# Kernel optimization log

Measured on AMD Instinct MI355X. Metric: run time of the kernel, lower is better.

Reference implementation:

```python
import jax, jax.numpy as jnp
import numpy as np

T, NP, NA, NV = 8, 16000, 16000, 200
DIN, H, KA, L = 256, 256, 4, 5
YEARS_TRAIN = (5, 6, 7)
BETA, EPS = 0.5, 1.0
SQRT2 = 1.4142135623730951


def setup_inputs() -> dict:
    key = jax.random.key(0)
    ks = jax.random.split(key, 24)
    s = 0.05
    return {
        'x_paper': jax.random.normal(ks[0], (T, NP, DIN), jnp.float32),
        'x_author': jax.random.normal(ks[1], (T, NA, DIN), jnp.float32),
        'x_venue': jax.random.normal(ks[2], (T, NV, DIN), jnp.float32),
        'neigh_author_idx': jax.random.randint(ks[3], (NP, KA), 0, NA),
        'neigh_venue_idx': jax.random.randint(ks[4], (NP,), 0, NV),
        'y_true': jax.random.uniform(ks[5], (len(YEARS_TRAIN), NP, L), jnp.float32, 0.0, 50.0),
        'W_paper': s * jax.random.normal(ks[6], (DIN, H), jnp.float32),
        'b_paper': jnp.zeros((H,), jnp.float32),
        'W_author': s * jax.random.normal(ks[7], (DIN, H), jnp.float32),
        'b_author': jnp.zeros((H,), jnp.float32),
        'W_venue': s * jax.random.normal(ks[8], (DIN, H), jnp.float32),
        'b_venue': jnp.zeros((H,), jnp.float32),
        'w_meta': jax.random.normal(ks[9], (3,), jnp.float32),
        'Wx': s * jax.random.normal(ks[10], (H, 3 * H), jnp.float32),
        'Wh': s * jax.random.normal(ks[11], (H, 3 * H), jnp.float32),
        'b_gru': jnp.zeros((3 * H,), jnp.float32),
        'W_eta': s * jax.random.normal(ks[12], (H, 1), jnp.float32),
        'b_eta': jnp.zeros((1,), jnp.float32),
        'W_mu': s * jax.random.normal(ks[13], (H, 1), jnp.float32),
        'b_mu': jnp.zeros((1,), jnp.float32),
        'W_sigma': s * jax.random.normal(ks[14], (H, 1), jnp.float32),
        'b_sigma': jnp.zeros((1,), jnp.float32),
    }


def reference(x_paper, x_author, x_venue, neigh_author_idx, neigh_venue_idx, y_true,
              W_paper, b_paper, W_author, b_author, W_venue, b_venue, w_meta,
              Wx, Wh, b_gru, W_eta, b_eta, W_mu, b_mu, W_sigma, b_sigma):
    # --- encoder: per-type linear + ReLU over all T snapshots ---
    emb_p = jax.nn.relu(jnp.einsum('tnd,dh->tnh', x_paper, W_paper) + b_paper)   # [T,NP,H]
    emb_a = jax.nn.relu(jnp.einsum('tnd,dh->tnh', x_author, W_author) + b_author)  # [T,NA,H]
    emb_v = jax.nn.relu(jnp.einsum('tnd,dh->tnh', x_venue, W_venue) + b_venue)   # [T,NV,H]

    # --- temporal smoothing regulariser L_time (all nodes common across years) ---
    l_time = jnp.mean(jnp.stack([
        jnp.mean(jnp.sum((e[1:] - e[:-1]) ** 2, axis=-1)) for e in (emb_p, emb_a, emb_v)
    ]))

    # --- weighted imputer, batched over all papers and all years ---
    w = jax.nn.softmax(w_meta)
    auth_mean = jnp.mean(emb_a[:, neigh_author_idx], axis=2)   # [T,NP,H]
    ven = emb_v[:, neigh_venue_idx]                            # [T,NP,H]
    v_all = w[0] * auth_mean + w[1] * ven + w[2] * emb_p       # [T,NP,H]

    # --- build lookback sequences V_p for all train years at once ---
    yrs = np.array([[t - k for k in range(1, L + 1)] for t in YEARS_TRAIN])  # [3,L]
    V = jnp.transpose(v_all[yrs], (0, 2, 1, 3)).reshape(-1, L, H)  # [B=3*NP, L, H]
    B = V.shape[0]

    # --- ImpactRNN: GRU over the lookback sequence ---
    def gru_step(h, x):
        gx = x @ Wx + b_gru
        gh = h @ Wh
        xr, xz, xn = jnp.split(gx, 3, axis=-1)
        hr, hz, hn = jnp.split(gh, 3, axis=-1)
        r = jax.nn.sigmoid(xr + hr)
        z = jax.nn.sigmoid(xz + hz)
        n = jnp.tanh(xn + r * hn)
        return (1.0 - z) * n + z * h, None

    h0 = jnp.zeros((B, H), V.dtype)
    h_last, _ = jax.lax.scan(gru_step, h0, jnp.swapaxes(V, 0, 1))

    eta = jax.nn.softplus(h_last @ W_eta + b_eta)              # [B,1]
    mu = h_last @ W_mu + b_mu                                  # [B,1]
    sigma = jax.nn.softplus(h_last @ W_sigma + b_sigma) + 1e-3  # [B,1]

    # --- cumulative log-normal citation curve, then per-horizon increments ---
    horizons = jnp.arange(1.0, L + 1.0, dtype=V.dtype)
    zscore = (jnp.log(horizons)[None, :] - mu) / (sigma * SQRT2)
    y_cum = eta * 0.5 * (1.0 + jax.lax.erf(zscore))            # [B,L]
    y_hat = jnp.concatenate([y_cum[:, :1], y_cum[:, 1:] - y_cum[:, :-1]], axis=1)

    l_pred = jnp.mean((jnp.log1p(y_true.reshape(-1, L) + EPS) - jnp.log1p(y_hat)) ** 2)
    return l_pred + BETA * l_time
```

## Files before the change

kernel.cpp:

```cpp
#include <hip/hip_runtime.h>
#include <cmath>

#define NP  16000
#define NV  200
#define HH  256

typedef short short8 __attribute__((ext_vector_type(8)));
typedef float f32x4  __attribute__((ext_vector_type(4)));

__device__ __forceinline__ unsigned short f2b(float f) {
  union { float f; unsigned u; } x; x.f = f;
  unsigned r = x.u + 0x7fffu + ((x.u >> 16) & 1u);
  return (unsigned short)(r >> 16);
}
__device__ __forceinline__ float b2f(unsigned short h) {
  union { unsigned u; float f; } x; x.u = ((unsigned)h) << 16;
  return x.f;
}
__device__ __forceinline__ float b2f_lo(unsigned u) {
  union { unsigned v; float f; } x; x.v = u << 16; return x.f;
}
__device__ __forceinline__ float b2f_hi(unsigned u) {
  union { unsigned v; float f; } x; x.v = u & 0xffff0000u; return x.f;
}
__device__ __forceinline__ unsigned cvt2(float a, float b) {
  unsigned r;
  asm("v_cvt_pk_bf16_f32 %0, %1, %2" : "=v"(r) : "v"(a), "v"(b));
  return r;
}
__device__ __forceinline__ void gld16(const void* g, void* l) {
  __builtin_amdgcn_global_load_lds((const __attribute__((address_space(1))) void*)g,
                                   (__attribute__((address_space(3))) void*)l, 16, 0, 0);
}
__device__ __forceinline__ float sigm(float x) { return 1.f / (1.f + __expf(-x)); }
__device__ __forceinline__ float tanhfast(float x) {
  const float e = __expf(-2.f * fabsf(x));
  const float t = (1.f - e) / (1.f + e);
  return x < 0.f ? -t : t;
}
__device__ __forceinline__ int xcd_swz(int orig, int q, int r) {
  const int xcd = orig & 7, loc = orig >> 3;
  return (xcd < r ? xcd * (q + 1) : r * (q + 1) + (xcd - r) * q) + loc;
}

__global__ __launch_bounds__(256) void packWt(const float* __restrict__ W,
                                              unsigned short* __restrict__ Wt) {
  const int n = blockIdx.x, k = threadIdx.x;
  Wt[n * 256 + k] = f2b(W[k * 256 + n]);
}
__global__ __launch_bounds__(256) void packW2t(const float* __restrict__ Wx,
                                               const float* __restrict__ Wh,
                                               unsigned short* __restrict__ W2t) {
  const int col = blockIdx.x;
  for (int k = threadIdx.x; k < 512; k += 256)
    W2t[(size_t)col * 512 + k] =
        f2b(k < 256 ? Wx[(size_t)k * 768 + col] : Wh[(size_t)(k - 256) * 768 + col]);
}

__global__ __launch_bounds__(256) void embed_f32(const float* __restrict__ Xf,
                                                 const unsigned short* __restrict__ Wt,
                                                 const float* __restrict__ bias,
                                                 unsigned short* __restrict__ E,
                                                 int M, int swq, int swr) {
  __shared__ __align__(16) unsigned short As[128 * 64];
  __shared__ __align__(16) unsigned short Bs[128 * 64];
  const int t = threadIdx.x, w = t >> 6, l = t & 63;
  const int work = xcd_swz(blockIdx.x, swq, swr);
  const int m0 = (work >> 1) * 128, n0 = (work & 1) * 128;
  const int srow = l >> 3;
  const int scol = ((l & 7) ^ srow) * 8;
  const f32x4 zero = {0.f, 0.f, 0.f, 0.f};
  f32x4 acc[4][4];
#pragma unroll
  for (int i = 0; i < 4; ++i)
#pragma unroll
    for (int j = 0; j < 4; ++j) acc[i][j] = zero;
  const int mrow0 = 64 * (w >> 1), ncol0 = 64 * (w & 1);

#pragma unroll
  for (int c = 0; c < 4; ++c) {
#pragma unroll
    for (int a = 0; a < 2; ++a) {
      const int idx = t * 2 + a;
      const int row = idx >> 2, cg = idx & 3;
      const int grow = min(m0 + row, M - 1);
      const float4* s = reinterpret_cast<const float4*>(Xf + (size_t)grow * 256 + c * 64 + cg * 16);
      const float4 f0 = s[0], f1 = s[1], f2 = s[2], f3 = s[3];
      uint4 u0, u1;
      u0.x = cvt2(f0.x, f0.y); u0.y = cvt2(f0.z, f0.w);
      u0.z = cvt2(f1.x, f1.y); u0.w = cvt2(f1.z, f1.w);
      u1.x = cvt2(f2.x, f2.y); u1.y = cvt2(f2.z, f2.w);
      u1.z = cvt2(f3.x, f3.y); u1.w = cvt2(f3.z, f3.w);
      const int s0 = (cg * 2) ^ (row & 7), s1 = (cg * 2 + 1) ^ (row & 7);
      *reinterpret_cast<uint4*>(As + row * 64 + s0 * 8) = u0;
      *reinterpret_cast<uint4*>(As + row * 64 + s1 * 8) = u1;
    }
#pragma unroll
    for (int i = 0; i < 4; ++i) {
      const int seg = 4 * w + i;
      gld16(Wt + (size_t)(n0 + 8 * seg + srow) * 256 + c * 64 + scol, (void*)(Bs + seg * 512));
    }
    __syncthreads();
#pragma unroll
    for (int ks = 0; ks < 2; ++ks) {
      short8 av[4], bv[4];
#pragma unroll
      for (int mi = 0; mi < 4; ++mi) {
        const int r = mrow0 + mi * 16 + (l & 15);
        const int slot = (ks * 4 + (l >> 4)) ^ (r & 7);
        av[mi] = *reinterpret_cast<const short8*>(As + r * 64 + slot * 8);
      }
#pragma unroll
      for (int nj = 0; nj < 4; ++nj) {
        const int r = ncol0 + nj * 16 + (l & 15);
        const int slot = (ks * 4 + (l >> 4)) ^ (r & 7);
        bv[nj] = *reinterpret_cast<const short8*>(Bs + r * 64 + slot * 8);
      }
#pragma unroll
      for (int mi = 0; mi < 4; ++mi)
#pragma unroll
        for (int nj = 0; nj < 4; ++nj)
          acc[mi][nj] = __builtin_amdgcn_mfma_f32_16x16x32_bf16(av[mi], bv[nj], acc[mi][nj], 0, 0, 0);
    }
    __syncthreads();
  }
#pragma unroll
  for (int nj = 0; nj < 4; ++nj) {
    const int colg = n0 + ncol0 + nj * 16 + (l & 15);
    const float bv = bias[colg];
#pragma unroll
    for (int mi = 0; mi < 4; ++mi) {
      const int rbase = m0 + mrow0 + mi * 16 + (l >> 4) * 4;
#pragma unroll
      for (int e = 0; e < 4; ++e) {
        const int row = rbase + e;
        if (row < M) E[(size_t)row * 256 + colg] = f2b(fmaxf(acc[mi][nj][e] + bv, 0.f));
      }
    }
  }
}

__global__ __launch_bounds__(256) void gx_gemm(const unsigned short* __restrict__ Abf,
                                               const unsigned short* __restrict__ W2t,
                                               const float* __restrict__ bias,
                                               unsigned short* __restrict__ GX) {
  __shared__ __align__(16) unsigned short As[128 * 64];
  __shared__ __align__(16) unsigned short Bs[128 * 64];
  const int t = threadIdx.x, w = t >> 6, l = t & 63;
  const int work = xcd_swz(blockIdx.x, 656, 2);
  const int m0 = (work / 6) * 128, n0 = (work % 6) * 128;
  const int srow = l >> 3;
  const int scol = ((l & 7) ^ srow) * 8;
  const f32x4 zero = {0.f, 0.f, 0.f, 0.f};
  f32x4 acc[4][4];
#pragma unroll
  for (int i = 0; i < 4; ++i)
#pragma unroll
    for (int j = 0; j < 4; ++j) acc[i][j] = zero;
  const int mrow0 = 64 * (w >> 1), ncol0 = 64 * (w & 1);

#pragma unroll
  for (int c = 0; c < 4; ++c) {
#pragma unroll
    for (int i = 0; i < 4; ++i) {
      const int seg = 4 * w + i;
      gld16(Abf + (size_t)(m0 + 8 * seg + srow) * 256 + c * 64 + scol, (void*)(As + seg * 512));
    }
#pragma unroll
    for (int i = 0; i < 4; ++i) {
      const int seg = 4 * w + i;
      gld16(W2t + (size_t)(n0 + 8 * seg + srow) * 512 + c * 64 + scol, (void*)(Bs + seg * 512));
    }
    __syncthreads();
#pragma unroll
    for (int ks = 0; ks < 2; ++ks) {
      short8 av[4], bv[4];
#pragma unroll
      for (int mi = 0; mi < 4; ++mi) {
        const int r = mrow0 + mi * 16 + (l & 15);
        const int slot = (ks * 4 + (l >> 4)) ^ (r & 7);
        av[mi] = *reinterpret_cast<const short8*>(As + r * 64 + slot * 8);
      }
#pragma unroll
      for (int nj = 0; nj < 4; ++nj) {
        const int r = ncol0 + nj * 16 + (l & 15);
        const int slot = (ks * 4 + (l >> 4)) ^ (r & 7);
        bv[nj] = *reinterpret_cast<const short8*>(Bs + r * 64 + slot * 8);
      }
#pragma unroll
      for (int mi = 0; mi < 4; ++mi)
#pragma unroll
        for (int nj = 0; nj < 4; ++nj)
          acc[mi][nj] = __builtin_amdgcn_mfma_f32_16x16x32_bf16(av[mi], bv[nj], acc[mi][nj], 0, 0, 0);
    }
    __syncthreads();
  }
#pragma unroll
  for (int nj = 0; nj < 4; ++nj) {
    const int colg = n0 + ncol0 + nj * 16 + (l & 15);
    const float bv = bias[colg];
#pragma unroll
    for (int mi = 0; mi < 4; ++mi) {
      const int rbase = m0 + mrow0 + mi * 16 + (l >> 4) * 4;
#pragma unroll
      for (int e = 0; e < 4; ++e)
        GX[(size_t)(rbase + e) * 768 + colg] = f2b(acc[mi][nj][e] + bv);
    }
  }
}

__global__ __launch_bounds__(256) void ltime_kernel(const unsigned short* __restrict__ ep,
                                                    const unsigned short* __restrict__ ea,
                                                    const unsigned short* __restrict__ ev,
                                                    float* __restrict__ partials) {
  const unsigned PO = 3584000u, VO = 44800u;
  const unsigned TOT = 2u * PO + VO;
  const unsigned SL = 512000u, SLV = 6400u;
  const float wbig = 1.f / (3.f * 7.f * 16000.f);
  const float wsmall = 1.f / (3.f * 7.f * 200.f);
  float local = 0.f;
  for (unsigned i = blockIdx.x * 256u + threadIdx.x; i < TOT; i += gridDim.x * 256u) {
    const unsigned short* base; unsigned off, sl; float wgt;
    if (i < 2u * PO) { base = (i < PO) ? ep : ea; off = (i < PO) ? i : i - PO; sl = SL; wgt = wbig; }
    else             { base = ev; off = i - 2u * PO; sl = SLV; wgt = wsmall; }
    const uint4 u0 = *reinterpret_cast<const uint4*>(base + (size_t)off * 8);
    const uint4 u1 = *reinterpret_cast<const uint4*>(base + (size_t)(off + sl) * 8);
    float s = 0.f, d;
    d = b2f_lo(u1.x) - b2f_lo(u0.x); s += d * d;
    d = b2f_hi(u1.x) - b2f_hi(u0.x); s += d * d;
    d = b2f_lo(u1.y) - b2f_lo(u0.y); s += d * d;
    d = b2f_hi(u1.y) - b2f_hi(u0.y); s += d * d;
    d = b2f_lo(u1.z) - b2f_lo(u0.z); s += d * d;
    d = b2f_hi(u1.z) - b2f_hi(u0.z); s += d * d;
    d = b2f_lo(u1.w) - b2f_lo(u0.w); s += d * d;
    d = b2f_hi(u1.w) - b2f_hi(u0.w); s += d * d;
    local += wgt * s;
  }
  __shared__ float red[256];
  red[threadIdx.x] = local;
  __syncthreads();
  for (int s = 128; s > 0; s >>= 1) {
    if (threadIdx.x < s) red[threadIdx.x] += red[threadIdx.x + s];
    __syncthreads();
  }
  if (threadIdx.x == 0) partials[blockIdx.x] = red[0];
}

__global__ __launch_bounds__(256) void vall_kernel(const unsigned short* __restrict__ ep,
                                                   const unsigned short* __restrict__ ea,
                                                   const unsigned short* __restrict__ ev,
                                                   const int* __restrict__ aidx,
                                                   const int* __restrict__ vidx,
                                                   const float* __restrict__ wm,
                                                   unsigned short* __restrict__ vall) {
  const int w = threadIdx.x >> 6, l = threadIdx.x & 63;
  const int n = blockIdx.x * 4 + w;
  float w0 = wm[0], w1 = wm[1], w2 = wm[2];
  const float mx = fmaxf(w0, fmaxf(w1, w2));
  const float e0 = expf(w0 - mx), e1 = expf(w1 - mx), e2 = expf(w2 - mx);
  const float inv = 1.f / (e0 + e1 + e2);
  w0 = e0 * inv; w1 = e1 * inv; w2 = e2 * inv;
  const int a0 = aidx[n * 4 + 0], a1 = aidx[n * 4 + 1];
  const int a2 = aidx[n * 4 + 2], a3 = aidx[n * 4 + 3];
  const int vn = vidx[n];
  const int cb = l * 4;
  for (int t = 0; t < 7; ++t) {
    const size_t tb = (size_t)t * NP * HH;
    const uint2 ua0 = *reinterpret_cast<const uint2*>(ea + tb + (size_t)a0 * HH + cb);
    const uint2 ua1 = *reinterpret_cast<const uint2*>(ea + tb + (size_t)a1 * HH + cb);
    const uint2 ua2 = *reinterpret_cast<const uint2*>(ea + tb + (size_t)a2 * HH + cb);
    const uint2 ua3 = *reinterpret_cast<const uint2*>(ea + tb + (size_t)a3 * HH + cb);
    const uint2 uv  = *reinterpret_cast<const uint2*>(ev + (size_t)t * NV * HH + (size_t)vn * HH + cb);
    const uint2 up  = *reinterpret_cast<const uint2*>(ep + tb + (size_t)n * HH + cb);
    float o[4];
    o[0] = w0 * 0.25f * (b2f_lo(ua0.x) + b2f_lo(ua1.x) + b2f_lo(ua2.x) + b2f_lo(ua3.x)) + w1 * b2f_lo(uv.x) + w2 * b2f_lo(up.x);
    o[1] = w0 * 0.25f * (b2f_hi(ua0.x) + b2f_hi(ua1.x) + b2f_hi(ua2.x) + b2f_hi(ua3.x)) + w1 * b2f_hi(uv.x) + w2 * b2f_hi(up.x);
    o[2] = w0 * 0.25f * (b2f_lo(ua0.y) + b2f_lo(ua1.y) + b2f_lo(ua2.y) + b2f_lo(ua3.y)) + w1 * b2f_lo(uv.y) + w2 * b2f_lo(up.y);
    o[3] = w0 * 0.25f * (b2f_hi(ua0.y) + b2f_hi(ua1.y) + b2f_hi(ua2.y) + b2f_hi(ua3.y)) + w1 * b2f_hi(uv.y) + w2 * b2f_hi(up.y);
    uint2 ov; ov.x = cvt2(o[0], o[1]); ov.y = cvt2(o[2], o[3]);
    *reinterpret_cast<uint2*>(vall + tb + (size_t)n * HH + cb) = ov;
  }
}

__global__ __launch_bounds__(256) void gru_h0(const unsigned short* __restrict__ GX,
                                              unsigned short* __restrict__ H0) {
  const int idx = blockIdx.x * 256 + threadIdx.x;
  const int hrow = idx >> 6, jq = idx & 63;
  const int g = (hrow >= 32000) ? 2 : (hrow >= 16000 ? 1 : 0);
  const int n = hrow - g * 16000;
  const size_t gxrow = (size_t)(4 + g) * 16000 + n;
  const unsigned short* gp = GX + gxrow * 768 + jq * 4;
  const uint2 uz = *reinterpret_cast<const uint2*>(gp + 256);
  const uint2 un = *reinterpret_cast<const uint2*>(gp + 512);
  float h[4];
  h[0] = (1.f - sigm(b2f_lo(uz.x))) * tanhfast(b2f_lo(un.x));
  h[1] = (1.f - sigm(b2f_hi(uz.x))) * tanhfast(b2f_hi(un.x));
  h[2] = (1.f - sigm(b2f_lo(uz.y))) * tanhfast(b2f_lo(un.y));
  h[3] = (1.f - sigm(b2f_hi(uz.y))) * tanhfast(b2f_hi(un.y));
  uint2 o; o.x = cvt2(h[0], h[1]); o.y = cvt2(h[2], h[3]);
  *reinterpret_cast<uint2*>(H0 + (size_t)hrow * 256 + jq * 4) = o;
}

__global__ __launch_bounds__(512) void gru_hstep(const unsigned short* __restrict__ GX,
                                                 const unsigned short* __restrict__ W2t,
                                                 const unsigned short* __restrict__ Hsrc,
                                                 unsigned short* __restrict__ Hdst,
                                                 int lstep) {
  __shared__ __align__(16) unsigned short As[128 * 64];
  __shared__ __align__(16) unsigned short Bs[384 * 64];
  const int t = threadIdx.x, w = t >> 6, l = t & 63;
  const int work = xcd_swz(blockIdx.x, 93, 6);
  const int bx = work >> 1, jb = work & 1;
  const int m0 = bx * 128, j0 = jb * 128;
  const int g = bx / 125;
  const size_t gxRowBase = (size_t)(4 + g - lstep) * 16000 + (size_t)(m0 - g * 16000);
  const int srow = l >> 3;
  const int scol = ((l & 7) ^ srow) * 8;
  const int wr = w >> 2, wj = w & 3;
  const f32x4 zero = {0.f, 0.f, 0.f, 0.f};
  f32x4 acc[3][4][2];
#pragma unroll
  for (int gate = 0; gate < 3; ++gate)
#pragma unroll
    for (int mi = 0; mi < 4; ++mi)
#pragma unroll
      for (int nj = 0; nj < 2; ++nj) acc[gate][mi][nj] = zero;

#pragma unroll
  for (int c = 0; c < 4; ++c) {
#pragma unroll
    for (int i = 0; i < 2; ++i) {
      const int seg = w * 2 + i;
      gld16(Hsrc + (size_t)(m0 + 8 * seg + srow) * 256 + c * 64 + scol, (void*)(As + seg * 512));
    }
#pragma unroll
    for (int i = 0; i < 6; ++i) {
      const int seg = w * 6 + i;
      const int tilerow = 8 * seg + srow;
      const int gate = tilerow >> 7, jj = tilerow & 127;
      gld16(W2t + (size_t)(gate * 256 + j0 + jj) * 512 + 256 + c * 64 + scol,
            (void*)(Bs + seg * 512));
    }
    __syncthreads();
#pragma unroll
    for (int ks = 0; ks < 2; ++ks) {
      short8 av[4], bv[6];
#pragma unroll
      for (int mi = 0; mi < 4; ++mi) {
        const int r = wr * 64 + mi * 16 + (l & 15);
        const int slot = (ks * 4 + (l >> 4)) ^ (r & 7);
        av[mi] = *reinterpret_cast<const short8*>(As + r * 64 + slot * 8);
      }
#pragma unroll
      for (int q = 0; q < 6; ++q) {
        const int r = (q >> 1) * 128 + wj * 32 + (q & 1) * 16 + (l & 15);
        const int slot = (ks * 4 + (l >> 4)) ^ (r & 7);
        bv[q] = *reinterpret_cast<const short8*>(Bs + r * 64 + slot * 8);
      }
#pragma unroll
      for (int gate = 0; gate < 3; ++gate)
#pragma unroll
        for (int mi = 0; mi < 4; ++mi)
#pragma unroll
          for (int nj = 0; nj < 2; ++nj)
            acc[gate][mi][nj] = __builtin_amdgcn_mfma_f32_16x16x32_bf16(
                av[mi], bv[gate * 2 + nj], acc[gate][mi][nj], 0, 0, 0);
    }
    __syncthreads();
  }
#pragma unroll
  for (int mi = 0; mi < 4; ++mi) {
#pragma unroll
    for (int nj = 0; nj < 2; ++nj) {
      const int jcol = j0 + wj * 32 + nj * 16 + (l & 15);
#pragma unroll
      for (int e = 0; e < 4; ++e) {
        const int rib = wr * 64 + mi * 16 + (l >> 4) * 4 + e;
        const size_t hidx = (size_t)(m0 + rib) * 256 + jcol;
        const size_t gxoff = (gxRowBase + rib) * 768 + jcol;
        const float aR = acc[0][mi][nj][e] + b2f(GX[gxoff]);
        const float aZ = acc[1][mi][nj][e] + b2f(GX[gxoff + 256]);
        const float hn = acc[2][mi][nj][e];
        const float xn = b2f(GX[gxoff + 512]);
        const float rg = sigm(aR);
        const float zg = sigm(aZ);
        const float ng = tanhfast(xn + rg * hn);
        const float ho = b2f(Hsrc[hidx]);
        Hdst[hidx] = f2b((1.f - zg) * ng + zg * ho);
      }
    }
  }
}

__device__ inline float softplusf(float x) { return x > 20.f ? x : log1pf(expf(x)); }

__global__ __launch_bounds__(256) void head_kernel(const unsigned short* __restrict__ Hbuf,
                                                   const float* __restrict__ We, const float* __restrict__ be,
                                                   const float* __restrict__ Wm, const float* __restrict__ bmu,
                                                   const float* __restrict__ Ws, const float* __restrict__ bsg,
                                                   const float* __restrict__ yt,
                                                   float* __restrict__ partials) {
  __shared__ float sWe[256], sWm[256], sWs[256];
  const int t = threadIdx.x;
  sWe[t] = We[t]; sWm[t] = Wm[t]; sWs[t] = Ws[t];
  __syncthreads();
  const int row = blockIdx.x * 256 + t;
  float loss = 0.f;
  if (row < 48000) {
    const unsigned short* h = Hbuf + (size_t)row * HH;
    float pe = 0.f, pm = 0.f, ps = 0.f;
#pragma unroll 4
    for (int k0 = 0; k0 < 256; k0 += 8) {
      const uint4 u = *reinterpret_cast<const uint4*>(h + k0);
      const float hv[8] = {b2f_lo(u.x), b2f_hi(u.x), b2f_lo(u.y), b2f_hi(u.y),
                           b2f_lo(u.z), b2f_hi(u.z), b2f_lo(u.w), b2f_hi(u.w)};
#pragma unroll
      for (int q = 0; q < 8; ++q) {
        const int k = k0 + q;
        pe += hv[q] * sWe[k]; pm += hv[q] * sWm[k]; ps += hv[q] * sWs[k];
      }
    }
    const float eta = softplusf(pe + be[0]);
    const float mu  = pm + bmu[0];
    const float sg  = softplusf(ps + bsg[0]) + 0.001f;
    const float inv = 1.f / (sg * 1.41421356237309515f);
    float prev = 0.f;
#pragma unroll
    for (int hz = 1; hz <= 5; ++hz) {
      const float z  = (logf((float)hz) - mu) * inv;
      const float yc = eta * 0.5f * (1.f + erff(z));
      const float yh = yc - prev; prev = yc;
      const float d  = log1pf(yt[(size_t)row * 5 + (hz - 1)] + 1.0f) - log1pf(yh);
      loss += d * d;
    }
  }
  __shared__ float red[256];
  red[t] = loss;
  __syncthreads();
  for (int s = 128; s > 0; s >>= 1) {
    if (t < s) red[t] += red[t + s];
    __syncthreads();
  }
  if (t == 0) partials[blockIdx.x] = red[0];
}

__global__ __launch_bounds__(256) void final_kernel(const float* __restrict__ lt,
                                                    const float* __restrict__ lp,
                                                    float* __restrict__ out) {
  __shared__ float r1[256], r2[256];
  float s1 = 0.f, s2 = 0.f;
  for (int i = threadIdx.x; i < 1024; i += 256) s1 += lt[i];
  for (int i = threadIdx.x; i < 188; i += 256) s2 += lp[i];
  r1[threadIdx.x] = s1; r2[threadIdx.x] = s2;
  __syncthreads();
  for (int s = 128; s > 0; s >>= 1) {
    if (threadIdx.x < s) { r1[threadIdx.x] += r1[threadIdx.x + s]; r2[threadIdx.x] += r2[threadIdx.x + s]; }
    __syncthreads();
  }
  if (threadIdx.x == 0) out[0] = r2[0] / 240000.f + 0.5f * r1[0];
}

extern "C" void kernel_launch(void* const* d_in, const int* in_sizes, int n_in,
                              void* d_out, int out_size, void* d_ws, size_t ws_size,
                              hipStream_t stream) {
  (void)in_sizes; (void)n_in; (void)out_size; (void)ws_size;
  const float* x_paper  = (const float*)d_in[0];
  const float* x_author = (const float*)d_in[1];
  const float* x_venue  = (const float*)d_in[2];
  const int*   aidx     = (const int*)d_in[3];
  const int*   vidx     = (const int*)d_in[4];
  const float* y_true   = (const float*)d_in[5];
  const float* W_paper  = (const float*)d_in[6];
  const float* b_paper  = (const float*)d_in[7];
  const float* W_author = (const float*)d_in[8];
  const float* b_author = (const float*)d_in[9];
  const float* W_venue  = (const float*)d_in[10];
  const float* b_venue  = (const float*)d_in[11];
  const float* w_meta   = (const float*)d_in[12];
  const float* Wx       = (const float*)d_in[13];
  const float* Wh       = (const float*)d_in[14];
  const float* b_gru    = (const float*)d_in[15];
  const float* W_eta    = (const float*)d_in[16];
  const float* b_eta    = (const float*)d_in[17];
  const float* W_mu     = (const float*)d_in[18];
  const float* b_mu     = (const float*)d_in[19];
  const float* W_sigma  = (const float*)d_in[20];
  const float* b_sigma  = (const float*)d_in[21];

  unsigned short* p = (unsigned short*)d_ws;
  unsigned short* va16 = p;  p += (size_t)7 * NP * 256;
  unsigned short* Hb0  = p;  p += (size_t)48000 * 256;
  unsigned short* Hb1  = p;  p += (size_t)48000 * 256;
  unsigned short* W2t  = p;  p += (size_t)768 * 512;
  unsigned short* GX   = p;  p += (size_t)112000 * 768;
  float* ltp = (float*)p;
  float* lpp = ltp + 1024;
  unsigned short* ep16 = GX;
  unsigned short* ea16 = ep16 + (size_t)8 * NP * 256;
  unsigned short* ev16 = ea16 + (size_t)8 * NP * 256;
  unsigned short* Wtp  = ev16 + (size_t)8 * NV * 256;
  unsigned short* Wta  = Wtp + 65536;
  unsigned short* Wtv  = Wta + 65536;

  packWt<<<256, 256, 0, stream>>>(W_paper,  Wtp);
  packWt<<<256, 256, 0, stream>>>(W_author, Wta);
  packWt<<<256, 256, 0, stream>>>(W_venue,  Wtv);
  packW2t<<<768, 256, 0, stream>>>(Wx, Wh, W2t);

  embed_f32<<<2000, 256, 0, stream>>>(x_paper,  Wtp, b_paper,  ep16, 8 * NP, 250, 0);
  embed_f32<<<2000, 256, 0, stream>>>(x_author, Wta, b_author, ea16, 8 * NP, 250, 0);
  embed_f32<<<26,   256, 0, stream>>>(x_venue,  Wtv, b_venue,  ev16, 8 * NV, 3, 2);

  ltime_kernel<<<1024, 256, 0, stream>>>(ep16, ea16, ev16, ltp);
  vall_kernel<<<NP / 4, 256, 0, stream>>>(ep16, ea16, ev16, aidx, vidx, w_meta, va16);

  gx_gemm<<<5250, 256, 0, stream>>>(va16, W2t, b_gru, GX);

  gru_h0<<<12000, 256, 0, stream>>>(GX, Hb0);
  gru_hstep<<<750, 512, 0, stream>>>(GX, W2t, Hb0, Hb1, 1);
  gru_hstep<<<750, 512, 0, stream>>>(GX, W2t, Hb1, Hb0, 2);
  gru_hstep<<<750, 512, 0, stream>>>(GX, W2t, Hb0, Hb1, 3);
  gru_hstep<<<750, 512, 0, stream>>>(GX, W2t, Hb1, Hb0, 4);

  head_kernel<<<188, 256, 0, stream>>>(Hb0, W_eta, b_eta, W_mu, b_mu, W_sigma, b_sigma,
                                       y_true, lpp);
  final_kernel<<<1, 256, 0, stream>>>(ltp, lpp, (float*)d_out);
}
```

Baseline: 613.6 us.

## Fuse three embedding GEMMs into one launch with full-width tiles and LDS-staged stores

The three per-type embedding GEMMs become a single 512-thread kernel launch. Each block now computes a full 128x256 output tile, so each input row is read and converted to bf16 only once instead of once per N-half, and the next A chunk is prefetched into registers while the current one is consumed. Epilogues in the embedding, gx_gemm and gru_hstep kernels now stage bf16 results in LDS and write them out as 16-byte row stores instead of scattered 2-byte stores. The GRU step loads its B fragments per gate to lower register pressure, and launch bounds request 4 waves per SIMD. The cost is extra LDS use, extra barriers in the epilogues, and the loss of XCD swizzling in the embedding kernel.

```diff
diff --git a/kernel.cpp b/kernel.cpp
--- a/kernel.cpp
+++ b/kernel.cpp
@@ -57,48 +57,64 @@
         f2b(k < 256 ? Wx[(size_t)k * 768 + col] : Wh[(size_t)(k - 256) * 768 + col]);
 }
 
-__global__ __launch_bounds__(256) void embed_f32(const float* __restrict__ Xf,
-                                                 const unsigned short* __restrict__ Wt,
-                                                 const float* __restrict__ bias,
-                                                 unsigned short* __restrict__ E,
-                                                 int M, int swq, int swr) {
-  __shared__ __align__(16) unsigned short As[128 * 64];
-  __shared__ __align__(16) unsigned short Bs[128 * 64];
+__global__ __launch_bounds__(512, 4) void embed_all(
+    const float* __restrict__ Xp, const float* __restrict__ Xa, const float* __restrict__ Xv,
+    const unsigned short* __restrict__ Wtp, const unsigned short* __restrict__ Wta,
+    const unsigned short* __restrict__ Wtv,
+    const float* __restrict__ bp, const float* __restrict__ ba, const float* __restrict__ bvn,
+    unsigned short* __restrict__ Ep, unsigned short* __restrict__ Ea,
+    unsigned short* __restrict__ Ev) {
+  __shared__ __align__(16) unsigned short lds[24576];
+  unsigned short* As = lds;
+  unsigned short* Bs = lds + 8192;
   const int t = threadIdx.x, w = t >> 6, l = t & 63;
-  const int work = xcd_swz(blockIdx.x, swq, swr);
-  const int m0 = (work >> 1) * 128, n0 = (work & 1) * 128;
-  const int srow = l >> 3;
-  const int scol = ((l & 7) ^ srow) * 8;
-  const f32x4 zero = {0.f, 0.f, 0.f, 0.f};
+  const int bid = blockIdx.x;
+  const float* Xf; const unsigned short* Wt; const float* bias; unsigned short* E;
+  int M, m0;
+  if (bid < 1000)      { Xf = Xp; Wt = Wtp; bias = bp;  E = Ep; M = 128000; m0 = bid * 128; }
+  else if (bid < 2000) { Xf = Xa; Wt = Wta; bias = ba;  E = Ea; M = 128000; m0 = (bid - 1000) * 128; }
+  else                 { Xf = Xv; Wt = Wtv; bias = bvn; E = Ev; M = 1600;   m0 = (bid - 2000) * 128; }
+  const int srow = l >> 3, scol = ((l & 7) ^ srow) * 8;
+  const int wr = w >> 2, wc = w & 3;
+  const int arow = t >> 2, acg = t & 3;
+  const int agrow = min(m0 + arow, M - 1);
+  const float* aptr = Xf + (size_t)agrow * 256 + acg * 16;
+
   f32x4 acc[4][4];
 #pragma unroll
   for (int i = 0; i < 4; ++i)
 #pragma unroll
-    for (int j = 0; j < 4; ++j) acc[i][j] = zero;
-  const int mrow0 = 64 * (w >> 1), ncol0 = 64 * (w & 1);
+    for (int j = 0; j < 4; ++j) acc[i][j] = {0.f, 0.f, 0.f, 0.f};
+
+  float4 areg0, areg1, areg2, areg3;
+  areg0 = *reinterpret_cast<const float4*>(aptr + 0);
+  areg1 = *reinterpret_cast<const float4*>(aptr + 4);
+  areg2 = *reinterpret_cast<const float4*>(aptr + 8);
+  areg3 = *reinterpret_cast<const float4*>(aptr + 12);
 
 #pragma unroll
   for (int c = 0; c < 4; ++c) {
-#pragma unroll
-    for (int a = 0; a < 2; ++a) {
-      const int idx = t * 2 + a;
-      const int row = idx >> 2, cg = idx & 3;
-      const int grow = min(m0 + row, M - 1);
-      const float4* s = reinterpret_cast<const float4*>(Xf + (size_t)grow * 256 + c * 64 + cg * 16);
-      const float4 f0 = s[0], f1 = s[1], f2 = s[2], f3 = s[3];
-      uint4 u0, u1;
-      u0.x = cvt2(f0.x, f0.y); u0.y = cvt2(f0.z, f0.w);
-      u0.z = cvt2(f1.x, f1.y); u0.w = cvt2(f1.z, f1.w);
-      u1.x = cvt2(f2.x, f2.y); u1.y = cvt2(f2.z, f2.w);
-      u1.z = cvt2(f3.x, f3.y); u1.w = cvt2(f3.z, f3.w);
-      const int s0 = (cg * 2) ^ (row & 7), s1 = (cg * 2 + 1) ^ (row & 7);
-      *reinterpret_cast<uint4*>(As + row * 64 + s0 * 8) = u0;
-      *reinterpret_cast<uint4*>(As + row * 64 + s1 * 8) = u1;
-    }
 #pragma unroll
     for (int i = 0; i < 4; ++i) {
       const int seg = 4 * w + i;
-      gld16(Wt + (size_t)(n0 + 8 * seg + srow) * 256 + c * 64 + scol, (void*)(Bs + seg * 512));
+      gld16(Wt + (size_t)(8 * seg + srow) * 256 + c * 64 + scol, (void*)(Bs + seg * 512));
+    }
+    {
+      uint4 u0, u1;
+      u0.x = cvt2(areg0.x, areg0.y); u0.y = cvt2(areg0.z, areg0.w);
+      u0.z = cvt2(areg1.x, areg1.y); u0.w = cvt2(areg1.z, areg1.w);
+      u1.x = cvt2(areg2.x, areg2.y); u1.y = cvt2(areg2.z, areg2.w);
+      u1.z = cvt2(areg3.x, areg3.y); u1.w = cvt2(areg3.z, areg3.w);
+      const int s0 = (acg * 2) ^ (arow & 7), s1 = (acg * 2 + 1) ^ (arow & 7);
+      *reinterpret_cast<uint4*>(As + arow * 64 + s0 * 8) = u0;
+      *reinterpret_cast<uint4*>(As + arow * 64 + s1 * 8) = u1;
+    }
+    if (c < 3) {
+      const float* np = aptr + (c + 1) * 64;
+      areg0 = *reinterpret_cast<const float4*>(np + 0);
+      areg1 = *reinterpret_cast<const float4*>(np + 4);
+      areg2 = *reinterpret_cast<const float4*>(np + 8);
+      areg3 = *reinterpret_cast<const float4*>(np + 12);
     }
     __syncthreads();
 #pragma unroll
@@ -106,13 +122,13 @@
       short8 av[4], bv[4];
 #pragma unroll
       for (int mi = 0; mi < 4; ++mi) {
-        const int r = mrow0 + mi * 16 + (l & 15);
+        const int r = wr * 64 + mi * 16 + (l & 15);
         const int slot = (ks * 4 + (l >> 4)) ^ (r & 7);
         av[mi] = *reinterpret_cast<const short8*>(As + r * 64 + slot * 8);
       }
 #pragma unroll
       for (int nj = 0; nj < 4; ++nj) {
-        const int r = ncol0 + nj * 16 + (l & 15);
+        const int r = wc * 64 + nj * 16 + (l & 15);
         const int slot = (ks * 4 + (l >> 4)) ^ (r & 7);
         bv[nj] = *reinterpret_cast<const short8*>(Bs + r * 64 + slot * 8);
       }
@@ -124,19 +140,33 @@
     }
     __syncthreads();
   }
-#pragma unroll
-  for (int nj = 0; nj < 4; ++nj) {
-    const int colg = n0 + ncol0 + nj * 16 + (l & 15);
-    const float bv = bias[colg];
-#pragma unroll
-    for (int mi = 0; mi < 4; ++mi) {
-      const int rbase = m0 + mrow0 + mi * 16 + (l >> 4) * 4;
-#pragma unroll
-      for (int e = 0; e < 4; ++e) {
-        const int row = rbase + e;
-        if (row < M) E[(size_t)row * 256 + colg] = f2b(fmaxf(acc[mi][nj][e] + bv, 0.f));
-      }
-    }
+
+  unsigned short* ep = lds + w * 2560;
+  const int grow = m0 + wr * 64 + l;
+#pragma unroll
+  for (int p = 0; p < 2; ++p) {
+#pragma unroll
+    for (int nj2 = 0; nj2 < 2; ++nj2) {
+      const int nj = 2 * p + nj2;
+      const int colg = wc * 64 + nj * 16 + (l & 15);
+      const float bvv = bias[colg];
+#pragma unroll
+      for (int mi = 0; mi < 4; ++mi)
+#pragma unroll
+        for (int e = 0; e < 4; ++e) {
+          const int rl = mi * 16 + (l >> 4) * 4 + e;
+          ep[rl * 40 + nj2 * 16 + (l & 15)] = f2b(fmaxf(acc[mi][nj][e] + bvv, 0.f));
+        }
+    }
+    __syncthreads();
+    if (grow < M) {
+#pragma unroll
+      for (int j = 0; j < 4; ++j) {
+        const uint4 v = *reinterpret_cast<const uint4*>(ep + l * 40 + j * 8);
+        *reinterpret_cast<uint4*>(E + (size_t)grow * 256 + wc * 64 + p * 32 + j * 8) = v;
+      }
+    }
+    __syncthreads();
   }
 }
 
@@ -144,19 +174,19 @@
                                                const unsigned short* __restrict__ W2t,
                                                const float* __restrict__ bias,
                                                unsigned short* __restrict__ GX) {
-  __shared__ __align__(16) unsigned short As[128 * 64];
-  __shared__ __align__(16) unsigned short Bs[128 * 64];
+  __shared__ __align__(16) unsigned short lds[16384];
+  unsigned short* As = lds;
+  unsigned short* Bs = lds + 8192;
   const int t = threadIdx.x, w = t >> 6, l = t & 63;
   const int work = xcd_swz(blockIdx.x, 656, 2);
   const int m0 = (work / 6) * 128, n0 = (work % 6) * 128;
   const int srow = l >> 3;
   const int scol = ((l & 7) ^ srow) * 8;
-  const f32x4 zero = {0.f, 0.f, 0.f, 0.f};
   f32x4 acc[4][4];
 #pragma unroll
   for (int i = 0; i < 4; ++i)
 #pragma unroll
-    for (int j = 0; j < 4; ++j) acc[i][j] = zero;
+    for (int j = 0; j < 4; ++j) acc[i][j] = {0.f, 0.f, 0.f, 0.f};
   const int mrow0 = 64 * (w >> 1), ncol0 = 64 * (w & 1);
 
 #pragma unroll
@@ -195,17 +225,30 @@
     }
     __syncthreads();
   }
-#pragma unroll
-  for (int nj = 0; nj < 4; ++nj) {
-    const int colg = n0 + ncol0 + nj * 16 + (l & 15);
-    const float bv = bias[colg];
-#pragma unroll
-    for (int mi = 0; mi < 4; ++mi) {
-      const int rbase = m0 + mrow0 + mi * 16 + (l >> 4) * 4;
-#pragma unroll
-      for (int e = 0; e < 4; ++e)
-        GX[(size_t)(rbase + e) * 768 + colg] = f2b(acc[mi][nj][e] + bv);
-    }
+  unsigned short* ep = lds + w * 2560;
+  const int grow = m0 + mrow0 + l;
+#pragma unroll
+  for (int p = 0; p < 2; ++p) {
+#pragma unroll
+    for (int nj2 = 0; nj2 < 2; ++nj2) {
+      const int nj = 2 * p + nj2;
+      const int colg = n0 + ncol0 + nj * 16 + (l & 15);
+      const float bvv = bias[colg];
+#pragma unroll
+      for (int mi = 0; mi < 4; ++mi)
+#pragma unroll
+        for (int e = 0; e < 4; ++e) {
+          const int rl = mi * 16 + (l >> 4) * 4 + e;
+          ep[rl * 40 + nj2 * 16 + (l & 15)] = f2b(acc[mi][nj][e] + bvv);
+        }
+    }
+    __syncthreads();
+#pragma unroll
+    for (int j = 0; j < 4; ++j) {
+      const uint4 v = *reinterpret_cast<const uint4*>(ep + l * 40 + j * 8);
+      *reinterpret_cast<uint4*>(GX + (size_t)grow * 768 + n0 + ncol0 + p * 32 + j * 8) = v;
+    }
+    __syncthreads();
   }
 }
 
@@ -301,13 +344,14 @@
   *reinterpret_cast<uint2*>(H0 + (size_t)hrow * 256 + jq * 4) = o;
 }
 
-__global__ __launch_bounds__(512) void gru_hstep(const unsigned short* __restrict__ GX,
-                                                 const unsigned short* __restrict__ W2t,
-                                                 const unsigned short* __restrict__ Hsrc,
-                                                 unsigned short* __restrict__ Hdst,
-                                                 int lstep) {
-  __shared__ __align__(16) unsigned short As[128 * 64];
-  __shared__ __align__(16) unsigned short Bs[384 * 64];
+__global__ __launch_bounds__(512, 4) void gru_hstep(const unsigned short* __restrict__ GX,
+                                                    const unsigned short* __restrict__ W2t,
+                                                    const unsigned short* __restrict__ Hsrc,
+                                                    unsigned short* __restrict__ Hdst,
+                                                    int lstep) {
+  __shared__ __align__(16) unsigned short lds[32768];
+  unsigned short* As = lds;
+  unsigned short* Bs = lds + 8192;
   const int t = threadIdx.x, w = t >> 6, l = t & 63;
   const int work = xcd_swz(blockIdx.x, 93, 6);
   const int bx = work >> 1, jb = work & 1;
@@ -317,14 +361,13 @@
   const int srow = l >> 3;
   const int scol = ((l & 7) ^ srow) * 8;
   const int wr = w >> 2, wj = w & 3;
-  const f32x4 zero = {0.f, 0.f, 0.f, 0.f};
   f32x4 acc[3][4][2];
 #pragma unroll
   for (int gate = 0; gate < 3; ++gate)
 #pragma unroll
     for (int mi = 0; mi < 4; ++mi)
 #pragma unroll
-      for (int nj = 0; nj < 2; ++nj) acc[gate][mi][nj] = zero;
+      for (int nj = 0; nj < 2; ++nj) acc[gate][mi][nj] = {0.f, 0.f, 0.f, 0.f};
 
 #pragma unroll
   for (int c = 0; c < 4; ++c) {
@@ -344,7 +387,7 @@
     __syncthreads();
 #pragma unroll
     for (int ks = 0; ks < 2; ++ks) {
-      short8 av[4], bv[6];
+      short8 av[4];
 #pragma unroll
       for (int mi = 0; mi < 4; ++mi) {
         const int r = wr * 64 + mi * 16 + (l & 15);
@@ -352,27 +395,31 @@
         av[mi] = *reinterpret_cast<const short8*>(As + r * 64 + slot * 8);
       }
 #pragma unroll
-      for (int q = 0; q < 6; ++q) {
-        const int r = (q >> 1) * 128 + wj * 32 + (q & 1) * 16 + (l & 15);
-        const int slot = (ks * 4 + (l >> 4)) ^ (r & 7);
-        bv[q] = *reinterpret_cast<const short8*>(Bs + r * 64 + slot * 8);
-      }
-#pragma unroll
-      for (int gate = 0; gate < 3; ++gate)
-#pragma unroll
-        for (int mi = 0; mi < 4; ++mi)
-#pragma unroll
-          for (int nj = 0; nj < 2; ++nj)
-            acc[gate][mi][nj] = __builtin_amdgcn_mfma_f32_16x16x32_bf16(
-                av[mi], bv[gate * 2 + nj], acc[gate][mi][nj], 0, 0, 0);
-    }
-    __syncthreads();
-  }
-#pragma unroll
-  for (int mi = 0; mi < 4; ++mi) {
-#pragma unroll
-    for (int nj = 0; nj < 2; ++nj) {
-      const int jcol = j0 + wj * 32 + nj * 16 + (l & 15);
+      for (int gate = 0; gate < 3; ++gate) {
+        short8 bv0, bv1;
+        {
+          const int r0 = gate * 128 + wj * 32 + (l & 15);
+          const int s0 = (ks * 4 + (l >> 4)) ^ (r0 & 7);
+          bv0 = *reinterpret_cast<const short8*>(Bs + r0 * 64 + s0 * 8);
+          const int r1 = r0 + 16;
+          const int s1 = (ks * 4 + (l >> 4)) ^ (r1 & 7);
+          bv1 = *reinterpret_cast<const short8*>(Bs + r1 * 64 + s1 * 8);
+        }
+#pragma unroll
+        for (int mi = 0; mi < 4; ++mi) {
+          acc[gate][mi][0] = __builtin_amdgcn_mfma_f32_16x16x32_bf16(av[mi], bv0, acc[gate][mi][0], 0, 0, 0);
+          acc[gate][mi][1] = __builtin_amdgcn_mfma_f32_16x16x32_bf16(av[mi], bv1, acc[gate][mi][1], 0, 0, 0);
+        }
+      }
+    }
+    __syncthreads();
+  }
+  unsigned short* ep = lds + w * 2560;
+#pragma unroll
+  for (int nj = 0; nj < 2; ++nj) {
+    const int jcol = j0 + wj * 32 + nj * 16 + (l & 15);
+#pragma unroll
+    for (int mi = 0; mi < 4; ++mi) {
 #pragma unroll
       for (int e = 0; e < 4; ++e) {
         const int rib = wr * 64 + mi * 16 + (l >> 4) * 4 + e;
@@ -386,8 +433,18 @@
         const float zg = sigm(aZ);
         const float ng = tanhfast(xn + rg * hn);
         const float ho = b2f(Hsrc[hidx]);
-        Hdst[hidx] = f2b((1.f - zg) * ng + zg * ho);
-      }
+        const int rl = mi * 16 + (l >> 4) * 4 + e;
+        ep[rl * 40 + nj * 16 + (l & 15)] = f2b((1.f - zg) * ng + zg * ho);
+      }
+    }
+  }
+  __syncthreads();
+  {
+    const int grow = m0 + wr * 64 + l;
+#pragma unroll
+    for (int j = 0; j < 4; ++j) {
+      const uint4 v = *reinterpret_cast<const uint4*>(ep + l * 40 + j * 8);
+      *reinterpret_cast<uint4*>(Hdst + (size_t)grow * 256 + j0 + wj * 32 + j * 8) = v;
     }
   }
 }
@@ -507,9 +564,8 @@
   packWt<<<256, 256, 0, stream>>>(W_venue,  Wtv);
   packW2t<<<768, 256, 0, stream>>>(Wx, Wh, W2t);
 
-  embed_f32<<<2000, 256, 0, stream>>>(x_paper,  Wtp, b_paper,  ep16, 8 * NP, 250, 0);
-  embed_f32<<<2000, 256, 0, stream>>>(x_author, Wta, b_author, ea16, 8 * NP, 250, 0);
-  embed_f32<<<26,   256, 0, stream>>>(x_venue,  Wtv, b_venue,  ev16, 8 * NV, 3, 2);
+  embed_all<<<2013, 512, 0, stream>>>(x_paper, x_author, x_venue, Wtp, Wta, Wtv,
+                                      b_paper, b_author, b_venue, ep16, ea16, ev16);
 
   ltime_kernel<<<1024, 256, 0, stream>>>(ep16, ea16, ev16, ltp);
   vall_kernel<<<NP / 4, 256, 0, stream>>>(ep16, ea16, ev16, aidx, vidx, w_meta, va16);
```

New measurement: 854.0 us. 1.39x slower.
